# Kernel tuning notes

Measured on AMD Instinct MI355X. Metric: run time of the kernel, lower is better.

The kernel has to match this reference:

```python
import jax, jax.numpy as jnp
import numpy as np
from jax import lax

# Inference-mode (training=False) ROIGenerator constants
PRE_NMS_TOPK = 1000
POST_NMS_TOPK = 1000
IOU_THRESHOLD = 0.7
SCORE_THRESHOLD = 0.0

LEVEL_SIZES = {2: 196608, 3: 49152, 4: 12288, 5: 3072}
BATCH = 8


def _make_boxes(key, shape):
    # valid yxyx boxes: y1 < y2, x1 < x2
    k1, k2 = jax.random.split(key)
    yx = jax.random.uniform(k1, shape[:-1] + (2,), dtype=jnp.float32) * 1000.0
    hw = jax.random.uniform(k2, shape[:-1] + (2,), dtype=jnp.float32) * 100.0 + 1.0
    return jnp.concatenate([yx, yx + hw], axis=-1)  # [B, N, 4] yxyx


def setup_inputs() -> dict:
    key = jax.random.key(0)
    ks = jax.random.split(key, 8)
    inp = {}
    for i, lvl in enumerate(sorted(LEVEL_SIZES)):
        n = LEVEL_SIZES[lvl]
        inp[f"boxes_p{lvl}"] = _make_boxes(ks[2 * i], (BATCH, n, 4))
        inp[f"scores_p{lvl}"] = jax.random.normal(ks[2 * i + 1], (BATCH, n), dtype=jnp.float32)
    return inp


def _pairwise_iou(b):
    # b: [B, K, 4] in yxyx -> iou: [B, K, K]
    y1, x1, y2, x2 = jnp.split(b, 4, axis=-1)           # each [B, K, 1]
    area = ((y2 - y1) * (x2 - x1))[..., 0]              # [B, K]
    iy1 = jnp.maximum(y1, jnp.swapaxes(y1, 1, 2))
    ix1 = jnp.maximum(x1, jnp.swapaxes(x1, 1, 2))
    iy2 = jnp.minimum(y2, jnp.swapaxes(y2, 1, 2))
    ix2 = jnp.minimum(x2, jnp.swapaxes(x2, 1, 2))
    ih = jnp.clip(iy2 - iy1, 0.0)
    iw = jnp.clip(ix2 - ix1, 0.0)
    inter = ih * iw                                     # [B, K, K]
    union = area[:, :, None] + area[:, None, :] - inter
    return jnp.where(union > 0, inter / union, 0.0)


def _per_level_gen(boxes, scores):
    # boxes: [B, N, 4] yxyx, scores: [B, N]
    n = scores.shape[1]
    pre_k = min(n, PRE_NMS_TOPK)
    post_k = min(n, POST_NMS_TOPK)

    s, idx = lax.top_k(scores, pre_k)                    # sorted desc, [B, pre_k]
    b = jnp.take_along_axis(boxes, idx[..., None], axis=1)  # [B, pre_k, 4]

    suppress = _pairwise_iou(b) > IOU_THRESHOLD          # [B, pre_k, pre_k]
    keep0 = s > SCORE_THRESHOLD                          # score filter
    ar = jnp.arange(pre_k)

    def step(i, keep):
        # box i suppressed if any earlier kept box overlaps it
        sup_i = jnp.any(suppress[:, :, i] & keep & (ar < i)[None, :], axis=1)
        return keep.at[:, i].set(keep[:, i] & ~sup_i)

    keep = lax.fori_loop(0, pre_k, step, keep0)          # [B, pre_k]

    # kept indices first (stable -> preserves score order), padded selection
    order = jnp.argsort((~keep).astype(jnp.int32), axis=1)  # jax argsort is stable
    sel = order[:, :post_k]                              # [B, post_k]
    num_valid = keep.sum(axis=1)                         # [B]

    level_rois = jnp.take_along_axis(b, sel[..., None], axis=1)   # [B, post_k, 4]
    level_scores = jnp.take_along_axis(s, sel, axis=1)            # [B, post_k]
    vmask = jnp.arange(post_k)[None, :] < num_valid[:, None]      # zero out padding
    level_rois = level_rois * vmask[..., None].astype(level_rois.dtype)
    level_scores = level_scores * vmask.astype(level_scores.dtype)
    return level_rois, level_scores


def _roi_generator(boxes_p2, boxes_p3, boxes_p4, boxes_p5,
                   scores_p2, scores_p3, scores_p4, scores_p5):
    levels = [(boxes_p2, scores_p2), (boxes_p3, scores_p3),
              (boxes_p4, scores_p4), (boxes_p5, scores_p5)]
    rois, roi_scores = [], []
    for b, s in levels:
        r, rs = _per_level_gen(b, s)
        rois.append(r)
        roi_scores.append(rs)
    rois = jnp.concatenate(rois, axis=1)                 # [B, 4*post_k, 4]
    roi_scores = jnp.concatenate(roi_scores, axis=1)     # [B, 4*post_k]
    overall_k = min(roi_scores.shape[1], POST_NMS_TOPK)
    roi_scores, sorted_idx = lax.top_k(roi_scores, overall_k)
    rois = jnp.take_along_axis(rois, sorted_idx[..., None], axis=1)
    return rois, roi_scores


def reference(boxes_p2, boxes_p3, boxes_p4, boxes_p5,
              scores_p2, scores_p3, scores_p4, scores_p5):
    return _roi_generator(boxes_p2, boxes_p3, boxes_p4, boxes_p5,
                          scores_p2, scores_p3, scores_p4, scores_p5)
```

## Files before the change

kernel.cpp:

```cpp
#include <hip/hip_runtime.h>

#define PRE_K 1000
#define CAP   2048
#define NBIN  8192
#define NB    1000
#define NW    16
#define TOT   4000
#define NLVL  4
#define BATCH 8
#define HB    8
#define MBM   16

__device__ __forceinline__ unsigned f2key(float f) {
    unsigned u = __float_as_uint(f);
    return (u & 0x80000000u) ? ~u : (u | 0x80000000u);
}
__device__ __forceinline__ float key2f(unsigned k) {
    unsigned u = (k & 0x80000000u) ? (k & 0x7FFFFFFFu) : ~k;
    return __uint_as_float(u);
}
__device__ __forceinline__ const float* lvl_scores(
    const float* s0, const float* s1, const float* s2, const float* s3, int lvl) {
    switch (lvl) { case 0: return s0; case 1: return s1; case 2: return s2; default: return s3; }
}
__device__ __forceinline__ const float* lvl_boxes(
    const float* b0, const float* b1, const float* b2, const float* b3, int lvl) {
    switch (lvl) { case 0: return b0; case 1: return b1; case 2: return b2; default: return b3; }
}
__device__ __forceinline__ int lvl_n(int lvl) {
    const int sizes[4] = {196608, 49152, 12288, 3072};
    return sizes[lvl];
}
__device__ __forceinline__ float bcast_f(float v, int i) {
    return __int_as_float(__builtin_amdgcn_readlane(__float_as_int(v), i));
}

__global__ __launch_bounds__(512) void init_kernel(
    unsigned* __restrict__ ghist, unsigned long long* __restrict__ ws_nz) {
    const int stride = gridDim.x * 512;
    for (int i = blockIdx.x * 512 + threadIdx.x; i < 32 * NBIN; i += stride)
        ghist[i] = 0u;
    for (int i = blockIdx.x * 512 + threadIdx.x; i < 32 * NW; i += stride)
        ws_nz[i] = 0ull;
}

__global__ __launch_bounds__(512) void hist_kernel(
    const float* __restrict__ scores0, const float* __restrict__ scores1,
    const float* __restrict__ scores2, const float* __restrict__ scores3,
    unsigned* __restrict__ ghist)
{
    const int blk = blockIdx.x / HB;
    const int hb  = blockIdx.x % HB;
    const int b   = blk >> 2;
    const int lvl = blk & 3;
    const int n   = lvl_n(lvl);
    const float* sc = lvl_scores(scores0, scores1, scores2, scores3, lvl) + (size_t)b * n;

    __shared__ unsigned lhist[2][NBIN];
    const int tid = threadIdx.x;
    const int rep = (tid >> 6) & 1;
    for (int i = tid; i < 2 * NBIN; i += 512) (&lhist[0][0])[i] = 0u;
    __syncthreads();

    const float4* sc4 = (const float4*)sc;
    const int n4 = n >> 2;
    for (int i = hb * 512 + tid; i < n4; i += HB * 512) {
        float4 v = sc4[i];
        atomicAdd(&lhist[rep][f2key(v.x) >> 19], 1u);
        atomicAdd(&lhist[rep][f2key(v.y) >> 19], 1u);
        atomicAdd(&lhist[rep][f2key(v.z) >> 19], 1u);
        atomicAdd(&lhist[rep][f2key(v.w) >> 19], 1u);
    }
    __syncthreads();

    unsigned* gh = ghist + (size_t)blk * NBIN;
    for (int i = tid; i < NBIN; i += 512) {
        unsigned v = lhist[0][i] + lhist[1][i];
        if (v) atomicAdd(&gh[i], v);
    }
}

__global__ __launch_bounds__(256) void select_kernel(
    const unsigned* __restrict__ ghist,
    unsigned* __restrict__ thresh,
    unsigned* __restrict__ counters)
{
    const int blk = blockIdx.x;
    const int tid = threadIdx.x;
    const unsigned* gh = ghist + (size_t)blk * NBIN;

    __shared__ unsigned csum[256];
    __shared__ int s_chunk;
    __shared__ unsigned s_before;

    unsigned s = 0;
    #pragma unroll 8
    for (int k = 0; k < 32; ++k) s += gh[tid * 32 + k];
    csum[tid] = s;
    __syncthreads();

    unsigned suf = 0;
    for (int c = tid + 1; c < 256; ++c) suf += csum[c];
    if (suf < PRE_K && suf + csum[tid] >= PRE_K) { s_chunk = tid; s_before = suf; }
    __syncthreads();

    if (tid == 0) {
        int C = s_chunk;
        unsigned acc = s_before;
        int T = C * 32;
        for (int bin = C * 32 + 31; bin >= C * 32; --bin) {
            acc += gh[bin];
            if (acc >= PRE_K) { T = bin; break; }
        }
        thresh[blk]   = (unsigned)T;
        counters[blk] = 0u;
    }
}

__global__ __launch_bounds__(512) void collect_kernel(
    const float* __restrict__ scores0, const float* __restrict__ scores1,
    const float* __restrict__ scores2, const float* __restrict__ scores3,
    const unsigned* __restrict__ thresh,
    unsigned* __restrict__ counters,
    unsigned long long* __restrict__ cand)
{
    const int blk = blockIdx.x / HB;
    const int hb  = blockIdx.x % HB;
    const int b   = blk >> 2;
    const int lvl = blk & 3;
    const int n   = lvl_n(lvl);
    const float* sc = lvl_scores(scores0, scores1, scores2, scores3, lvl) + (size_t)b * n;
    const unsigned T = thresh[blk];
    unsigned long long* candp = cand + (size_t)blk * CAP;

    __shared__ unsigned long long cbuf[CAP];
    __shared__ unsigned ccnt, cbase;

    const int tid  = threadIdx.x;
    const int lane = tid & 63;
    if (tid == 0) ccnt = 0;
    __syncthreads();

    for (int i = hb * 512 + tid; i < n; i += HB * 512) {
        unsigned key = f2key(sc[i]);
        bool pred = (key >> 19) >= T;
        unsigned long long act = __ballot(pred);
        if (act) {
            int leader = __ffsll((long long)act) - 1;
            unsigned base = 0;
            if (lane == leader) base = atomicAdd(&ccnt, (unsigned)__popcll(act));
            base = __shfl(base, leader, 64);
            if (pred) {
                unsigned pos = base + (unsigned)__popcll(act & ((1ull << lane) - 1ull));
                if (pos < CAP)
                    cbuf[pos] = ((unsigned long long)key << 32) | (unsigned)(~i);
            }
        }
    }
    __syncthreads();
    unsigned cnt = ccnt; if (cnt > CAP) cnt = CAP;
    if (tid == 0) cbase = atomicAdd(&counters[blk], cnt);
    __syncthreads();
    const unsigned gb = cbase;
    for (unsigned i = tid; i < cnt; i += 512) {
        unsigned p = gb + i;
        if (p < CAP) candp[p] = cbuf[i];
    }
}

__global__ __launch_bounds__(1024) void sortemit_kernel(
    const float* __restrict__ boxes0, const float* __restrict__ boxes1,
    const float* __restrict__ boxes2, const float* __restrict__ boxes3,
    const unsigned* __restrict__ counters,
    const unsigned long long* __restrict__ cand,
    float* __restrict__ ws_scores,
    float* __restrict__ ws_boxes)
{
    const int blk = blockIdx.x;
    const int b   = blk >> 2;
    const int lvl = blk & 3;
    const int n   = lvl_n(lvl);
    const float* bx = lvl_boxes(boxes0, boxes1, boxes2, boxes3, lvl) + (size_t)b * n * 4;
    const unsigned long long* candp = cand + (size_t)blk * CAP;

    __shared__ unsigned long long arr[CAP];
    const int tid = threadIdx.x;
    unsigned cnt = counters[blk]; if (cnt > CAP) cnt = CAP;

    for (int i = tid; i < CAP; i += 1024)
        arr[i] = (i < (int)cnt) ? candp[i] : 0ull;
    __syncthreads();

    for (unsigned kk = 2; kk <= CAP; kk <<= 1) {
        for (unsigned j = kk >> 1; j > 0; j >>= 1) {
            for (unsigned i = tid; i < CAP; i += 1024) {
                unsigned p = i ^ j;
                if (p > i) {
                    unsigned long long a = arr[i], c = arr[p];
                    bool desc = ((i & kk) == 0);
                    if (desc ? (a < c) : (a > c)) { arr[i] = c; arr[p] = a; }
                }
            }
            __syncthreads();
        }
    }

    for (int r = tid; r < PRE_K; r += 1024) {
        unsigned long long c = arr[r];
        unsigned key = (unsigned)(c >> 32);
        int idx = (int)(~(unsigned)c);
        ws_scores[(size_t)blk * PRE_K + r] = key2f(key);
        float* dst = ws_boxes + ((size_t)blk * PRE_K + r) * 4;
        const float* src = bx + (size_t)idx * 4;
        dst[0] = src[0]; dst[1] = src[1]; dst[2] = src[2]; dst[3] = src[3];
    }
}

__global__ __launch_bounds__(256) void mask_kernel(
    const float* __restrict__ ws_boxes,
    unsigned long long* __restrict__ ws_mask,
    unsigned long long* __restrict__ ws_nz)
{
    const int blk  = blockIdx.x / MBM;
    const int mb   = blockIdx.x % MBM;
    const int tid  = threadIdx.x;
    const int lane = tid & 63;
    const int wv   = tid >> 6;

    __shared__ float4 sbox[1024];

    const float4* bxp = (const float4*)(ws_boxes + (size_t)blk * NB * 4);
    for (int i = tid; i < 1024; i += 256)
        sbox[i] = (i < NB) ? bxp[i] : make_float4(0.f, 0.f, 0.f, 0.f);
    __syncthreads();

    unsigned long long* maskp = ws_mask + (size_t)blk * NB * NW;
    unsigned long long* nzp   = ws_nz + (size_t)blk * NW;
    const double CSUM = (double)__uint_as_float(0x3F333333u)
                      + (double)__uint_as_float(0x3F333334u);

    for (int t = mb * 4 + wv; t < 136; t += MBM * 4) {
        int w = 0, acc = 0;
        while (acc + w + 1 <= t) { acc += w + 1; ++w; }
        const int rb = t - acc;
        const int rbase = rb * 64;

        const float4 rbx = sbox[rbase + lane];
        const float   ra = (rbx.z - rbx.x) * (rbx.w - rbx.y);
        const float4 cbx = sbox[w * 64 + lane];
        const float   ca = (cbx.z - cbx.x) * (cbx.w - cbx.y);

        unsigned long long myw = 0ull;
        #pragma unroll
        for (int jj = 0; jj < 64; ++jj) {
            const float cy1 = bcast_f(cbx.x, jj);
            const float cx1 = bcast_f(cbx.y, jj);
            const float cy2 = bcast_f(cbx.z, jj);
            const float cx2 = bcast_f(cbx.w, jj);
            const float caj = bcast_f(ca, jj);
            float iy1 = fmaxf(rbx.x, cy1);
            float ix1 = fmaxf(rbx.y, cx1);
            float iy2 = fminf(rbx.z, cy2);
            float ix2 = fminf(rbx.w, cx2);
            float ih = fmaxf(iy2 - iy1, 0.0f);
            float iw = fmaxf(ix2 - ix1, 0.0f);
            float inter = ih * iw;
            float uni = ra + caj - inter;
            bool pred = (uni > 0.0f) &&
                        (2.0 * (double)inter >= CSUM * (double)uni);
            myw |= ((unsigned long long)pred) << jj;
        }
        if (w == rb)
            myw &= ~((2ull << lane) - 1ull);
        if (rbase + lane < NB)
            maskp[(size_t)(rbase + lane) * NW + w] = myw;
        unsigned long long nzb = __ballot(myw != 0ull);
        if (lane == 0 && nzb) atomicOr(&nzp[rb], nzb);
    }
}

__global__ __launch_bounds__(1024) void greedy_kernel(
    float* __restrict__ ws_scores,
    float* __restrict__ ws_boxes,
    const unsigned long long* __restrict__ ws_mask,
    const unsigned long long* __restrict__ ws_nz)
{
    const int blk  = blockIdx.x;
    const int tid  = threadIdx.x;
    const int lane = tid & 63;
    const int wv   = tid >> 6;

    __shared__ unsigned long long Mrow[NB * NW];
    __shared__ float4 sbox[NB];
    __shared__ float  ssc[NB];
    __shared__ unsigned long long nzlds[NW];
    __shared__ unsigned long long keepw[NW];
    __shared__ int wprefix[NW];
    __shared__ int slist[NB];
    __shared__ int sL;

    float* scp = ws_scores + (size_t)blk * NB;
    float* bxp = ws_boxes  + (size_t)blk * NB * 4;
    const unsigned long long* mrows = ws_mask + (size_t)blk * NB * NW;

    if (tid < NW) nzlds[tid] = ws_nz[(size_t)blk * NW + tid];
    for (int i = tid; i < NB; i += 1024) {
        sbox[i] = ((const float4*)bxp)[i];
        ssc[i]  = scp[i];
    }
    {
        const int j = wv * 64 + lane;
        bool pred = (j < NB) && (scp[j] > 0.0f);
        unsigned long long bal = __ballot(pred);
        if (lane == 0) keepw[wv] = bal;
    }
    __syncthreads();

    if (tid == 0) {
        int L = 0;
        for (int c = 0; c < NW; ++c) {
            unsigned long long p = nzlds[c];
            while (p) {
                int i = __ffsll((long long)p) - 1;
                slist[L++] = c * 64 + i;
                p &= p - 1;
            }
        }
        sL = L;
    }
    __syncthreads();
    const int L = sL;

    for (int idx = tid; idx < L * NW; idx += 1024) {
        int r = slist[idx >> 4];
        Mrow[idx] = mrows[(size_t)r * NW + (idx & 15)];
    }
    __syncthreads();

    if (tid < 64) {
        unsigned long long kp = (lane < NW) ? keepw[lane] : 0ull;
        unsigned long long mnext = (L > 0 && lane < NW) ? Mrow[lane] : 0ull;
        int rnext = (L > 0) ? slist[0] : 0;
        for (int k = 0; k < L; ++k) {
            unsigned long long m = mnext;
            const int r = rnext;
            if (k + 1 < L) {
                rnext = slist[k + 1];
                mnext = (lane < NW) ? Mrow[(size_t)(k + 1) * NW + lane] : 0ull;
            }
            const int c = r >> 6;
            unsigned klo = (unsigned)__builtin_amdgcn_readlane((int)(unsigned)kp, c);
            unsigned khi = (unsigned)__builtin_amdgcn_readlane((int)(unsigned)(kp >> 32), c);
            unsigned long long kw = ((unsigned long long)khi << 32) | klo;
            if ((kw >> (r & 63)) & 1ull) {
                unsigned long long mm = (lane >= c) ? m : 0ull;
                kp &= ~mm;
            }
        }
        if (lane < NW) keepw[lane] = kp;
    }
    __syncthreads();
    if (tid == 0) {
        int acc = 0;
        for (int w = 0; w < NW; ++w) { wprefix[w] = acc; acc += __popcll(keepw[w]); }
    }
    __syncthreads();

    for (int i = tid; i < NB; i += 1024) scp[i] = 0.0f;
    for (int i = tid; i < NB * 4; i += 1024) bxp[i] = 0.0f;
    __syncthreads();
    for (int i = tid; i < NB; i += 1024) {
        const int w = i >> 6;
        const unsigned long long kw = keepw[w];
        if ((kw >> (i & 63)) & 1ull) {
            int rank = wprefix[w] + __popcll(kw & ((1ull << (i & 63)) - 1ull));
            scp[rank] = ssc[i];
            float4 bb = sbox[i];
            float* dst = bxp + (size_t)rank * 4;
            dst[0] = bb.x; dst[1] = bb.y; dst[2] = bb.z; dst[3] = bb.w;
        }
    }
}

__global__ __launch_bounds__(1024) void final_merge_kernel(
    const float* __restrict__ ws_scores,
    const float* __restrict__ ws_boxes,
    float* __restrict__ out)
{
    const int blk = blockIdx.x;
    const int b   = blk >> 2;
    const int lvl = blk & 3;
    const int tid = threadIdx.x;

    __shared__ unsigned long long lists[NLVL][PRE_K];

    for (int i = tid; i < TOT; i += 1024) {
        unsigned u = f2key(ws_scores[(size_t)b * TOT + i]);
        lists[i / PRE_K][i % PRE_K] =
            ((unsigned long long)u << 32) | (unsigned)(~i);
    }
    __syncthreads();

    float* out_rois   = out;
    float* out_scores = out + 32000;

    for (int r = tid; r < PRE_K; r += 1024) {
        const unsigned long long c = lists[lvl][r];
        int rank = r;
        #pragma unroll
        for (int l = 0; l < NLVL; ++l) {
            if (l == lvl) continue;
            int lo = 0, hi = PRE_K;
            while (lo < hi) {
                int mid = (lo + hi) >> 1;
                if (lists[l][mid] > c) lo = mid + 1; else hi = mid;
            }
            rank += lo;
        }
        if (rank < PRE_K) {
            out_scores[(size_t)b * PRE_K + rank] = key2f((unsigned)(c >> 32));
            const int pos = lvl * PRE_K + r;
            const float4 bb = ((const float4*)ws_boxes)[(size_t)b * TOT + pos];
            float* dst = out_rois + ((size_t)b * PRE_K + rank) * 4;
            dst[0] = bb.x; dst[1] = bb.y; dst[2] = bb.z; dst[3] = bb.w;
        }
    }
}

extern "C" void kernel_launch(void* const* d_in, const int* in_sizes, int n_in,
                              void* d_out, int out_size, void* d_ws, size_t ws_size,
                              hipStream_t stream) {
    const float* boxes0  = (const float*)d_in[0];
    const float* scores0 = (const float*)d_in[1];
    const float* boxes1  = (const float*)d_in[2];
    const float* scores1 = (const float*)d_in[3];
    const float* boxes2  = (const float*)d_in[4];
    const float* scores2 = (const float*)d_in[5];
    const float* boxes3  = (const float*)d_in[6];
    const float* scores3 = (const float*)d_in[7];
    float* out = (float*)d_out;

    char* base = (char*)d_ws;
    float* ws_scores = (float*)base;
    float* ws_boxes  = (float*)(base + 128000);
    unsigned long long* ws_mask = (unsigned long long*)(base + 640000);
    unsigned long long* ws_nz   = (unsigned long long*)(base + 4736000);
    unsigned long long* cand = (unsigned long long*)(base + 640000);
    unsigned* ghist    = (unsigned*)(base + 1164288);
    unsigned* counters = (unsigned*)(base + 2212864);
    unsigned* thresh   = (unsigned*)(base + 2212992);

    init_kernel<<<128, 512, 0, stream>>>(ghist, ws_nz);
    hist_kernel<<<BATCH * NLVL * HB, 512, 0, stream>>>(
        scores0, scores1, scores2, scores3, ghist);
    select_kernel<<<BATCH * NLVL, 256, 0, stream>>>(ghist, thresh, counters);
    collect_kernel<<<BATCH * NLVL * HB, 512, 0, stream>>>(
        scores0, scores1, scores2, scores3, thresh, counters, cand);
    sortemit_kernel<<<BATCH * NLVL, 1024, 0, stream>>>(
        boxes0, boxes1, boxes2, boxes3, counters, cand, ws_scores, ws_boxes);
    mask_kernel<<<BATCH * NLVL * MBM, 256, 0, stream>>>(ws_boxes, ws_mask, ws_nz);
    greedy_kernel<<<BATCH * NLVL, 1024, 0, stream>>>(ws_scores, ws_boxes, ws_mask, ws_nz);
    final_merge_kernel<<<BATCH * NLVL, 1024, 0, stream>>>(ws_scores, ws_boxes, out);
}
```

Before: 110.4 us.

## Drop init and select kernels; per-block partial histograms reduced inside collect

Removes the zero-init kernel by clearing counters and ws_nz inside hist_kernel. Each histogram block now writes its own partial histogram with plain stores instead of global atomics. The threshold selection moves from a separate select kernel into collect_kernel, where every block sums the HB partials and finds the threshold redundantly. This cuts two launches and the global atomics, but each collect block repeats the reduction and needs more shared memory and a larger workspace.

```diff
diff --git a/kernel.cpp b/kernel.cpp
--- a/kernel.cpp
+++ b/kernel.cpp
@@ -35,19 +35,12 @@
     return __int_as_float(__builtin_amdgcn_readlane(__float_as_int(v), i));
 }
 
-__global__ __launch_bounds__(512) void init_kernel(
-    unsigned* __restrict__ ghist, unsigned long long* __restrict__ ws_nz) {
-    const int stride = gridDim.x * 512;
-    for (int i = blockIdx.x * 512 + threadIdx.x; i < 32 * NBIN; i += stride)
-        ghist[i] = 0u;
-    for (int i = blockIdx.x * 512 + threadIdx.x; i < 32 * NW; i += stride)
-        ws_nz[i] = 0ull;
-}
-
 __global__ __launch_bounds__(512) void hist_kernel(
     const float* __restrict__ scores0, const float* __restrict__ scores1,
     const float* __restrict__ scores2, const float* __restrict__ scores3,
-    unsigned* __restrict__ ghist)
+    unsigned* __restrict__ ghist,
+    unsigned* __restrict__ counters,
+    unsigned long long* __restrict__ ws_nz)
 {
     const int blk = blockIdx.x / HB;
     const int hb  = blockIdx.x % HB;
@@ -60,6 +53,10 @@
     const int tid = threadIdx.x;
     const int rep = (tid >> 6) & 1;
     for (int i = tid; i < 2 * NBIN; i += 512) (&lhist[0][0])[i] = 0u;
+    if (hb == 0) {
+        if (tid == 0) counters[blk] = 0u;
+        if (tid < NW) ws_nz[(size_t)blk * NW + tid] = 0ull;
+    }
     __syncthreads();
 
     const float4* sc4 = (const float4*)sc;
@@ -73,54 +70,15 @@
     }
     __syncthreads();
 
-    unsigned* gh = ghist + (size_t)blk * NBIN;
-    for (int i = tid; i < NBIN; i += 512) {
-        unsigned v = lhist[0][i] + lhist[1][i];
-        if (v) atomicAdd(&gh[i], v);
-    }
-}
-
-__global__ __launch_bounds__(256) void select_kernel(
-    const unsigned* __restrict__ ghist,
-    unsigned* __restrict__ thresh,
-    unsigned* __restrict__ counters)
-{
-    const int blk = blockIdx.x;
-    const int tid = threadIdx.x;
-    const unsigned* gh = ghist + (size_t)blk * NBIN;
-
-    __shared__ unsigned csum[256];
-    __shared__ int s_chunk;
-    __shared__ unsigned s_before;
-
-    unsigned s = 0;
-    #pragma unroll 8
-    for (int k = 0; k < 32; ++k) s += gh[tid * 32 + k];
-    csum[tid] = s;
-    __syncthreads();
-
-    unsigned suf = 0;
-    for (int c = tid + 1; c < 256; ++c) suf += csum[c];
-    if (suf < PRE_K && suf + csum[tid] >= PRE_K) { s_chunk = tid; s_before = suf; }
-    __syncthreads();
-
-    if (tid == 0) {
-        int C = s_chunk;
-        unsigned acc = s_before;
-        int T = C * 32;
-        for (int bin = C * 32 + 31; bin >= C * 32; --bin) {
-            acc += gh[bin];
-            if (acc >= PRE_K) { T = bin; break; }
-        }
-        thresh[blk]   = (unsigned)T;
-        counters[blk] = 0u;
-    }
+    unsigned* gh = ghist + ((size_t)blk * HB + hb) * NBIN;
+    for (int i = tid; i < NBIN; i += 512)
+        gh[i] = lhist[0][i] + lhist[1][i];
 }
 
 __global__ __launch_bounds__(512) void collect_kernel(
     const float* __restrict__ scores0, const float* __restrict__ scores1,
     const float* __restrict__ scores2, const float* __restrict__ scores3,
-    const unsigned* __restrict__ thresh,
+    const unsigned* __restrict__ ghist,
     unsigned* __restrict__ counters,
     unsigned long long* __restrict__ cand)
 {
@@ -130,16 +88,53 @@
     const int lvl = blk & 3;
     const int n   = lvl_n(lvl);
     const float* sc = lvl_scores(scores0, scores1, scores2, scores3, lvl) + (size_t)b * n;
-    const unsigned T = thresh[blk];
     unsigned long long* candp = cand + (size_t)blk * CAP;
 
+    __shared__ unsigned hsum[NBIN];
+    __shared__ unsigned csum[256];
+    __shared__ int s_chunk;
+    __shared__ unsigned s_before, sT;
     __shared__ unsigned long long cbuf[CAP];
     __shared__ unsigned ccnt, cbase;
 
     const int tid  = threadIdx.x;
     const int lane = tid & 63;
     if (tid == 0) ccnt = 0;
-    __syncthreads();
+
+    for (int i = tid; i < NBIN; i += 512) {
+        unsigned v = 0;
+        #pragma unroll
+        for (int p = 0; p < HB; ++p)
+            v += ghist[((size_t)blk * HB + p) * NBIN + i];
+        hsum[i] = v;
+    }
+    __syncthreads();
+    if (tid < 256) {
+        unsigned s = 0;
+        #pragma unroll
+        for (int k = 0; k < 32; ++k)
+            s += hsum[tid * 32 + ((k + tid) & 31)];
+        csum[tid] = s;
+    }
+    __syncthreads();
+    if (tid < 256) {
+        unsigned suf = 0;
+        for (int c = tid + 1; c < 256; ++c) suf += csum[c];
+        if (suf < PRE_K && suf + csum[tid] >= PRE_K) { s_chunk = tid; s_before = suf; }
+    }
+    __syncthreads();
+    if (tid == 0) {
+        int C = s_chunk;
+        unsigned acc = s_before;
+        int T = C * 32;
+        for (int bin = C * 32 + 31; bin >= C * 32; --bin) {
+            acc += hsum[bin];
+            if (acc >= PRE_K) { T = bin; break; }
+        }
+        sT = (unsigned)T;
+    }
+    __syncthreads();
+    const unsigned T = sT;
 
     for (int i = hb * 512 + tid; i < n; i += HB * 512) {
         unsigned key = f2key(sc[i]);
@@ -445,17 +440,14 @@
     float* ws_boxes  = (float*)(base + 128000);
     unsigned long long* ws_mask = (unsigned long long*)(base + 640000);
     unsigned long long* ws_nz   = (unsigned long long*)(base + 4736000);
-    unsigned long long* cand = (unsigned long long*)(base + 640000);
-    unsigned* ghist    = (unsigned*)(base + 1164288);
-    unsigned* counters = (unsigned*)(base + 2212864);
-    unsigned* thresh   = (unsigned*)(base + 2212992);
-
-    init_kernel<<<128, 512, 0, stream>>>(ghist, ws_nz);
+    unsigned long long* cand    = (unsigned long long*)(base + 4740096);
+    unsigned* ghist             = (unsigned*)(base + 5264384);
+    unsigned* counters          = (unsigned*)(base + 13652992);
+
     hist_kernel<<<BATCH * NLVL * HB, 512, 0, stream>>>(
-        scores0, scores1, scores2, scores3, ghist);
-    select_kernel<<<BATCH * NLVL, 256, 0, stream>>>(ghist, thresh, counters);
+        scores0, scores1, scores2, scores3, ghist, counters, ws_nz);
     collect_kernel<<<BATCH * NLVL * HB, 512, 0, stream>>>(
-        scores0, scores1, scores2, scores3, thresh, counters, cand);
+        scores0, scores1, scores2, scores3, ghist, counters, cand);
     sortemit_kernel<<<BATCH * NLVL, 1024, 0, stream>>>(
         boxes0, boxes1, boxes2, boxes3, counters, cand, ws_scores, ws_boxes);
     mask_kernel<<<BATCH * NLVL * MBM, 256, 0, stream>>>(ws_boxes, ws_mask, ws_nz);
```

Measured after the change: 114.6 us. +3.8%, slower.

## Fold threshold selection into collect kernel and double mask kernel blocks

Applied to the files above, without the earlier changes.

Removes the separate select kernel: each collect block now recomputes the per-level top-k histogram threshold redundantly from the global histogram before filtering, eliminating one launch and the thresh buffer. Counter zeroing moves into the init kernel, and the candidate/histogram buffers are relocated so they no longer alias the mask region. The mask kernel grid is doubled (MBM 16 to 32) for more parallelism, and init uses more blocks. Redundant threshold computation across 8 blocks per level adds some extra histogram reads.

```diff
diff --git a/kernel.cpp b/kernel.cpp
--- a/kernel.cpp
+++ b/kernel.cpp
@@ -9,7 +9,7 @@
 #define NLVL  4
 #define BATCH 8
 #define HB    8
-#define MBM   16
+#define MBM   32
 
 __device__ __forceinline__ unsigned f2key(float f) {
     unsigned u = __float_as_uint(f);
@@ -36,12 +36,15 @@
 }
 
 __global__ __launch_bounds__(512) void init_kernel(
-    unsigned* __restrict__ ghist, unsigned long long* __restrict__ ws_nz) {
+    unsigned* __restrict__ ghist, unsigned* __restrict__ counters,
+    unsigned long long* __restrict__ ws_nz) {
     const int stride = gridDim.x * 512;
     for (int i = blockIdx.x * 512 + threadIdx.x; i < 32 * NBIN; i += stride)
         ghist[i] = 0u;
-    for (int i = blockIdx.x * 512 + threadIdx.x; i < 32 * NW; i += stride)
-        ws_nz[i] = 0ull;
+    if (blockIdx.x == 0) {
+        if (threadIdx.x < 32) counters[threadIdx.x] = 0u;
+        for (int i = threadIdx.x; i < 32 * NW; i += 512) ws_nz[i] = 0ull;
+    }
 }
 
 __global__ __launch_bounds__(512) void hist_kernel(
@@ -80,30 +83,45 @@
     }
 }
 
-__global__ __launch_bounds__(256) void select_kernel(
+__global__ __launch_bounds__(512) void collect_kernel(
+    const float* __restrict__ scores0, const float* __restrict__ scores1,
+    const float* __restrict__ scores2, const float* __restrict__ scores3,
     const unsigned* __restrict__ ghist,
-    unsigned* __restrict__ thresh,
-    unsigned* __restrict__ counters)
-{
-    const int blk = blockIdx.x;
-    const int tid = threadIdx.x;
+    unsigned* __restrict__ counters,
+    unsigned long long* __restrict__ cand)
+{
+    const int blk = blockIdx.x / HB;
+    const int hb  = blockIdx.x % HB;
+    const int b   = blk >> 2;
+    const int lvl = blk & 3;
+    const int n   = lvl_n(lvl);
+    const float* sc = lvl_scores(scores0, scores1, scores2, scores3, lvl) + (size_t)b * n;
     const unsigned* gh = ghist + (size_t)blk * NBIN;
+    unsigned long long* candp = cand + (size_t)blk * CAP;
 
     __shared__ unsigned csum[256];
     __shared__ int s_chunk;
-    __shared__ unsigned s_before;
-
-    unsigned s = 0;
-    #pragma unroll 8
-    for (int k = 0; k < 32; ++k) s += gh[tid * 32 + k];
-    csum[tid] = s;
-    __syncthreads();
-
-    unsigned suf = 0;
-    for (int c = tid + 1; c < 256; ++c) suf += csum[c];
-    if (suf < PRE_K && suf + csum[tid] >= PRE_K) { s_chunk = tid; s_before = suf; }
-    __syncthreads();
-
+    __shared__ unsigned s_before, sT;
+    __shared__ unsigned long long cbuf[CAP];
+    __shared__ unsigned ccnt, cbase;
+
+    const int tid  = threadIdx.x;
+    const int lane = tid & 63;
+    if (tid == 0) ccnt = 0;
+
+    if (tid < 256) {
+        unsigned s = 0;
+        #pragma unroll 8
+        for (int k = 0; k < 32; ++k) s += gh[tid * 32 + k];
+        csum[tid] = s;
+    }
+    __syncthreads();
+    if (tid < 256) {
+        unsigned suf = 0;
+        for (int c = tid + 1; c < 256; ++c) suf += csum[c];
+        if (suf < PRE_K && suf + csum[tid] >= PRE_K) { s_chunk = tid; s_before = suf; }
+    }
+    __syncthreads();
     if (tid == 0) {
         int C = s_chunk;
         unsigned acc = s_before;
@@ -112,34 +130,10 @@
             acc += gh[bin];
             if (acc >= PRE_K) { T = bin; break; }
         }
-        thresh[blk]   = (unsigned)T;
-        counters[blk] = 0u;
-    }
-}
-
-__global__ __launch_bounds__(512) void collect_kernel(
-    const float* __restrict__ scores0, const float* __restrict__ scores1,
-    const float* __restrict__ scores2, const float* __restrict__ scores3,
-    const unsigned* __restrict__ thresh,
-    unsigned* __restrict__ counters,
-    unsigned long long* __restrict__ cand)
-{
-    const int blk = blockIdx.x / HB;
-    const int hb  = blockIdx.x % HB;
-    const int b   = blk >> 2;
-    const int lvl = blk & 3;
-    const int n   = lvl_n(lvl);
-    const float* sc = lvl_scores(scores0, scores1, scores2, scores3, lvl) + (size_t)b * n;
-    const unsigned T = thresh[blk];
-    unsigned long long* candp = cand + (size_t)blk * CAP;
-
-    __shared__ unsigned long long cbuf[CAP];
-    __shared__ unsigned ccnt, cbase;
-
-    const int tid  = threadIdx.x;
-    const int lane = tid & 63;
-    if (tid == 0) ccnt = 0;
-    __syncthreads();
+        sT = (unsigned)T;
+    }
+    __syncthreads();
+    const unsigned T = sT;
 
     for (int i = hb * 512 + tid; i < n; i += HB * 512) {
         unsigned key = f2key(sc[i]);
@@ -445,17 +439,15 @@
     float* ws_boxes  = (float*)(base + 128000);
     unsigned long long* ws_mask = (unsigned long long*)(base + 640000);
     unsigned long long* ws_nz   = (unsigned long long*)(base + 4736000);
-    unsigned long long* cand = (unsigned long long*)(base + 640000);
-    unsigned* ghist    = (unsigned*)(base + 1164288);
-    unsigned* counters = (unsigned*)(base + 2212864);
-    unsigned* thresh   = (unsigned*)(base + 2212992);
-
-    init_kernel<<<128, 512, 0, stream>>>(ghist, ws_nz);
+    unsigned long long* cand    = (unsigned long long*)(base + 4740096);
+    unsigned* ghist             = (unsigned*)(base + 5264384);
+    unsigned* counters          = (unsigned*)(base + 6312960);
+
+    init_kernel<<<256, 512, 0, stream>>>(ghist, counters, ws_nz);
     hist_kernel<<<BATCH * NLVL * HB, 512, 0, stream>>>(
         scores0, scores1, scores2, scores3, ghist);
-    select_kernel<<<BATCH * NLVL, 256, 0, stream>>>(ghist, thresh, counters);
     collect_kernel<<<BATCH * NLVL * HB, 512, 0, stream>>>(
-        scores0, scores1, scores2, scores3, thresh, counters, cand);
+        scores0, scores1, scores2, scores3, ghist, counters, cand);
     sortemit_kernel<<<BATCH * NLVL, 1024, 0, stream>>>(
         boxes0, boxes1, boxes2, boxes3, counters, cand, ws_scores, ws_boxes);
     mask_kernel<<<BATCH * NLVL * MBM, 256, 0, stream>>>(ws_boxes, ws_mask, ws_nz);
```

New measurement: 115.2 us. 4.3% more time.
